# Performance work log

Hardware: AMD Instinct MI355X
Metric: run time of the kernel (lower is better)

The kernel has to match this reference:

```python
import jax, jax.numpy as jnp
import numpy as np

B, N, D, E = 256, 192, 512, 1024
H = E // 2          # MLP hidden = 512
K = 58              # round(0.3 * 192), hardcoded in the torch forward
EPS_L2 = 1e-8
EPS_BN = 1e-5


def setup_inputs() -> dict:
    key = jax.random.key(0)
    ks = jax.random.split(key, 8)
    s = 0.02
    return {
        "all_patch_embeddings": jax.random.normal(ks[0], (B, N, D), dtype=jnp.float32),
        "attention_map": jax.random.uniform(ks[1], (B, N + 1, N + 1), dtype=jnp.float32),
        # fc: Linear(D, E)
        "W_fc": jax.random.normal(ks[2], (E, D), dtype=jnp.float32) * s,
        "b_fc": jnp.zeros((E,), dtype=jnp.float32),
        # mlp layer 0: Linear(D, H) + BatchNorm1d(H) + ReLU
        "W1": jax.random.normal(ks[3], (H, D), dtype=jnp.float32) * s,
        "b1": jnp.zeros((H,), dtype=jnp.float32),
        "gamma1": jnp.ones((H,), dtype=jnp.float32),
        "beta1": jnp.zeros((H,), dtype=jnp.float32),
        # mlp layer 1: Linear(H, E) (no BN/ReLU applied on last layer)
        "W2": jax.random.normal(ks[4], (E, H), dtype=jnp.float32) * s,
        "b2": jnp.zeros((E,), dtype=jnp.float32),
    }


def reference(all_patch_embeddings, attention_map, W_fc, b_fc, W1, b1, gamma1, beta1, W2, b2):
    # CLS-row attention over the 192 patch tokens: [B, N]
    cls_attn = attention_map[:, 0, 1:]
    # torch.sort(descending)[...,:K] == top-k indices (batched, replaces python loop)
    _, idx = jax.lax.top_k(cls_attn, K)                      # [B, K] int32
    # batched gather replacing the per-sample index_select loop
    sel = jnp.take_along_axis(all_patch_embeddings, idx[:, :, None], axis=1)  # [B, K, D]
    # l2norm over last dim
    norm = jnp.sqrt(jnp.sum(sel * sel, axis=-1, keepdims=True)) + EPS_L2
    base = sel / norm
    # .half() cast in the original (round-trip to fp16 precision)
    base = base.astype(jnp.float16).astype(jnp.float32)
    # fc branch
    feat_fc = jnp.einsum('bkd,ed->bke', base, W_fc) + b_fc    # [B, K, E]
    # mlp branch (num_layers=2): Linear -> BN(train-mode batch stats) -> ReLU -> Linear
    h = jnp.einsum('bkd,hd->bkh', base, W1) + b1              # [B, K, H]
    hf = h.reshape(B * K, H)
    mu = jnp.mean(hf, axis=0)
    var = jnp.var(hf, axis=0)
    hf = (hf - mu) * jax.lax.rsqrt(var + EPS_BN) * gamma1 + beta1
    h = jax.nn.relu(hf).reshape(B, K, H)
    feat_mlp = jnp.einsum('bkh,eh->bke', h, W2) + b2          # [B, K, E]
    feats = feat_mlp + feat_fc
    # maxk_pool1d_var with k=1 and lengths == K reduces to max over token dim
    return jnp.max(feats, axis=1).astype(jnp.float32)         # [B, E]
```

## Files before the change

kernel.cpp:

```cpp
#include <hip/hip_runtime.h>
#include <hip/hip_fp16.h>

#define B_ 256
#define N_ 192
#define D_ 512
#define E_ 1024
#define H_ 512
#define K_ 58
#define M_ (B_*K_)
#define M2_ (B_*64)

typedef _Float16 f16;
typedef unsigned int u32;
typedef _Float16 half8 __attribute__((ext_vector_type(8)));
typedef float floatx4 __attribute__((ext_vector_type(4)));

__device__ inline half8 cvt8(float4 f0, float4 f1) {
  half8 r;
  r[0]=(f16)f0.x; r[1]=(f16)f0.y; r[2]=(f16)f0.z; r[3]=(f16)f0.w;
  r[4]=(f16)f1.x; r[5]=(f16)f1.y; r[6]=(f16)f1.z; r[7]=(f16)f1.w;
  return r;
}

__device__ inline void gl_lds16(const f16* g, f16* l) {
  __builtin_amdgcn_global_load_lds((const __attribute__((address_space(1))) u32*)g,
                                   (__attribute__((address_space(3))) u32*)l, 16, 0, 0);
}

__device__ inline void stage128(const f16* gbase, int gstride, f16* sT, int w, int lane) {
  int lrow  = lane >> 2;
  int chunk = (lane & 3) ^ ((lane >> 3) & 3);
  gl_lds16(gbase + (size_t)(w*16      + lrow)*gstride + chunk*8, &sT[(w*16)*32]);
  gl_lds16(gbase + (size_t)(64 + w*16 + lrow)*gstride + chunk*8, &sT[(64 + w*16)*32]);
}

__global__ void setup_kernel(const float* __restrict__ Wfc, const float* __restrict__ W2,
                             const float* __restrict__ W1, const float* __restrict__ attn,
                             const float* __restrict__ emb,
                             f16* __restrict__ Wcat, f16* __restrict__ W1_16,
                             f16* __restrict__ A16, float* __restrict__ csum) {
  __shared__ float sv[N_];
  __shared__ int sidx[K_];
  __shared__ int cnt;
  int blk = blockIdx.x, t = threadIdx.x;
  if (blk < 512) {
    int idx = (blk*256 + t)*8;
    int e = idx >> 10, c = idx & 1023;
    const float* src = (c < 512) ? (Wfc + (size_t)e*512 + c)
                                 : (W2  + (size_t)e*512 + (c-512));
    half8 o = cvt8(((const float4*)src)[0], ((const float4*)src)[1]);
    *(uint4*)(Wcat + idx) = *(uint4*)&o;
  } else if (blk < 640) {
    int idx = ((blk-512)*256 + t)*8;
    const float* src = W1 + idx;
    half8 o = cvt8(((const float4*)src)[0], ((const float4*)src)[1]);
    *(uint4*)(W1_16 + idx) = *(uint4*)&o;
  } else if (blk < 896) {
    int b = blk - 640;
    if (t == 0) cnt = 0;
    if (t < N_) sv[t] = attn[(size_t)b*193*193 + 1 + t];
    __syncthreads();
    if (t < N_) {
      float v = sv[t]; int rank = 0;
      for (int j = 0; j < N_; ++j) {
        float vj = sv[j];
        rank += (vj > v) || (vj == v && j < t);
      }
      if (rank < K_) sidx[atomicAdd(&cnt, 1)] = t;
    }
    __syncthreads();
    int w = t >> 6, lane = t & 63;
    for (int slot = w; slot < 64; slot += 4) {
      f16* dst = A16 + ((size_t)b*64 + slot)*1024 + lane*8;
      if (slot < K_) {
        const float* src = emb + ((size_t)b*N_ + sidx[slot])*D_ + lane*8;
        float4 v0 = ((const float4*)src)[0];
        float4 v1 = ((const float4*)src)[1];
        float s = v0.x*v0.x + v0.y*v0.y + v0.z*v0.z + v0.w*v0.w
                + v1.x*v1.x + v1.y*v1.y + v1.z*v1.z + v1.w*v1.w;
        #pragma unroll
        for (int off = 32; off > 0; off >>= 1) s += __shfl_xor(s, off);
        float inv = 1.0f / (sqrtf(s) + 1e-8f);
        half8 o;
        o[0]=(f16)(v0.x*inv); o[1]=(f16)(v0.y*inv); o[2]=(f16)(v0.z*inv); o[3]=(f16)(v0.w*inv);
        o[4]=(f16)(v1.x*inv); o[5]=(f16)(v1.y*inv); o[6]=(f16)(v1.z*inv); o[7]=(f16)(v1.w*inv);
        *(uint4*)dst = *(uint4*)&o;
      } else {
        uint4 z; z.x=0u; z.y=0u; z.z=0u; z.w=0u;
        *(uint4*)dst = z;
      }
    }
  } else {
    float4 z; z.x=0.f; z.y=0.f; z.z=0.f; z.w=0.f;
    ((float4*)csum)[t] = z;
  }
}

__launch_bounds__(256)
__global__ void gemm1_kernel(const f16* __restrict__ A16, const f16* __restrict__ W1_16,
                             const float* __restrict__ b1, f16* __restrict__ Aout,
                             float* __restrict__ csum, float* __restrict__ css) {
  __shared__ f16 sA[128*32];
  __shared__ f16 sB[128*32];
  __shared__ float sSum[4][64], sSS[4][64];
  int t = threadIdx.x;
  int n0 = blockIdx.x * 128;
  int m0 = blockIdx.y * 128;
  int lane = t & 63, w = t >> 6, lm = lane & 15, quad = lane >> 4;
  int rh = w & 1, ch = w >> 1;
  floatx4 acc[4][4] = {};
  const f16* Ab = A16 + (size_t)m0*1024;
  const f16* Bb = W1_16 + (size_t)n0*512;
  int sw = (quad ^ ((lm >> 1) & 3)) * 8;
  for (int k0 = 0; k0 < 512; k0 += 32) {
    stage128(Ab + k0, 1024, sA, w, lane);
    stage128(Bb + k0, 512,  sB, w, lane);
    __syncthreads();
    half8 a[4], bf[4];
    #pragma unroll
    for (int i = 0; i < 4; ++i) a[i]  = *(const half8*)&sA[(rh*64 + i*16 + lm)*32 + sw];
    #pragma unroll
    for (int j = 0; j < 4; ++j) bf[j] = *(const half8*)&sB[(ch*64 + j*16 + lm)*32 + sw];
    #pragma unroll
    for (int i = 0; i < 4; ++i)
      #pragma unroll
      for (int j = 0; j < 4; ++j)
        acc[i][j] = __builtin_amdgcn_mfma_f32_16x16x32_f16(a[i], bf[j], acc[i][j], 0, 0, 0);
    __syncthreads();
  }
  #pragma unroll
  for (int j = 0; j < 4; ++j) {
    int col = n0 + ch*64 + j*16 + lm;
    float bias = b1[col];
    float s = 0.f, ss = 0.f;
    #pragma unroll
    for (int i = 0; i < 4; ++i) {
      int rib = i*16 + quad*4;
      int row = m0 + rh*64 + rib;
      #pragma unroll
      for (int r = 0; r < 4; ++r) {
        float x = acc[i][j][r] + bias;
        Aout[(size_t)(row + r)*1024 + 512 + col] = (f16)x;
        if (rib + r < K_) { s += x; ss += x*x; }
      }
    }
    s  += __shfl_xor(s, 16);  s  += __shfl_xor(s, 32);
    ss += __shfl_xor(ss, 16); ss += __shfl_xor(ss, 32);
    if (lane < 16) { sSum[w][j*16 + lm] = s; sSS[w][j*16 + lm] = ss; }
  }
  __syncthreads();
  if (t < 128) {
    int wp = (t >> 6) * 2, ci = t & 63;
    atomicAdd(&csum[n0 + t], sSum[wp][ci] + sSum[wp+1][ci]);
    atomicAdd(&css[n0 + t],  sSS[wp][ci]  + sSS[wp+1][ci]);
  }
}

__global__ void bnrelu_kernel(f16* __restrict__ A16, const float* __restrict__ csum,
                              const float* __restrict__ css, const float* __restrict__ gamma,
                              const float* __restrict__ beta) {
  __shared__ float sSc[H_], sSh[H_];
  int t = threadIdx.x;
  for (int j = t; j < H_; j += 256) {
    float mu  = csum[j] * (1.0f/M_);
    float var = css[j] * (1.0f/M_) - mu*mu;
    float sc  = gamma[j] * rsqrtf(var + 1e-5f);
    sSc[j] = sc;
    sSh[j] = beta[j] - mu*sc;
  }
  __syncthreads();
  int r0 = blockIdx.x * 16;
  #pragma unroll
  for (int i = 0; i < 4; ++i) {
    int seg = t + 256*i;
    int row = r0 + (seg >> 6);
    int c0  = (seg & 63) * 8;
    f16* p = A16 + (size_t)row*1024 + 512 + c0;
    if ((row & 63) >= K_) {
      uint4 z; z.x=0u; z.y=0u; z.z=0u; z.w=0u;
      *(uint4*)p = z;
    } else {
      half8 hv = *(const half8*)p;
      half8 o;
      #pragma unroll
      for (int k = 0; k < 8; ++k)
        o[k] = (f16)fmaxf((float)hv[k]*sSc[c0+k] + sSh[c0+k], 0.0f);
      *(uint4*)p = *(uint4*)&o;
    }
  }
}

__launch_bounds__(256)
__global__ void fused_kernel(const f16* __restrict__ A16, const f16* __restrict__ Wcat,
                             const float* __restrict__ bfc, const float* __restrict__ b2,
                             float* __restrict__ out) {
  __shared__ f16 sA[128*32];
  __shared__ f16 sB[128*32];
  __shared__ float sMax[4][64];
  int t = threadIdx.x;
  int e0 = blockIdx.x * 128;
  int bm = blockIdx.y;
  int lane = t & 63, w = t >> 6, lm = lane & 15, quad = lane >> 4;
  int rh = w & 1, ch = w >> 1;
  floatx4 acc[4][4] = {};
  const f16* Ab = A16 + (size_t)bm*128*1024;
  const f16* Bb = Wcat + (size_t)e0*1024;
  int sw = (quad ^ ((lm >> 1) & 3)) * 8;
  for (int k0 = 0; k0 < 1024; k0 += 32) {
    stage128(Ab + k0, 1024, sA, w, lane);
    stage128(Bb + k0, 1024, sB, w, lane);
    __syncthreads();
    half8 a[4], bf[4];
    #pragma unroll
    for (int i = 0; i < 4; ++i) a[i]  = *(const half8*)&sA[(rh*64 + i*16 + lm)*32 + sw];
    #pragma unroll
    for (int j = 0; j < 4; ++j) bf[j] = *(const half8*)&sB[(ch*64 + j*16 + lm)*32 + sw];
    #pragma unroll
    for (int i = 0; i < 4; ++i)
      #pragma unroll
      for (int j = 0; j < 4; ++j)
        acc[i][j] = __builtin_amdgcn_mfma_f32_16x16x32_f16(a[i], bf[j], acc[i][j], 0, 0, 0);
    __syncthreads();
  }
  #pragma unroll
  for (int j = 0; j < 4; ++j) {
    float mx = -3.0e38f;
    #pragma unroll
    for (int i = 0; i < 4; ++i) {
      int rib = i*16 + quad*4;
      #pragma unroll
      for (int r = 0; r < 4; ++r)
        if (rib + r < K_) mx = fmaxf(mx, acc[i][j][r]);
    }
    mx = fmaxf(mx, __shfl_xor(mx, 16));
    mx = fmaxf(mx, __shfl_xor(mx, 32));
    if (lane < 16) sMax[w][j*16 + lm] = mx;
  }
  __syncthreads();
  {
    int bb = t >> 7, c = t & 127;
    float mx = sMax[(c >> 6)*2 + bb][c & 63];
    int e = e0 + c;
    out[((size_t)bm*2 + bb)*E_ + e] = mx + bfc[e] + b2[e];
  }
}

extern "C" void kernel_launch(void* const* d_in, const int* in_sizes, int n_in,
                              void* d_out, int out_size, void* d_ws, size_t ws_size,
                              hipStream_t stream) {
  const float* emb   = (const float*)d_in[0];
  const float* attn  = (const float*)d_in[1];
  const float* Wfc   = (const float*)d_in[2];
  const float* bfc   = (const float*)d_in[3];
  const float* W1    = (const float*)d_in[4];
  const float* b1    = (const float*)d_in[5];
  const float* gamma = (const float*)d_in[6];
  const float* beta  = (const float*)d_in[7];
  const float* W2    = (const float*)d_in[8];
  const float* b2    = (const float*)d_in[9];
  float* out = (float*)d_out;

  char* ws = (char*)d_ws;
  f16*   A16   = (f16*)(ws);
  f16*   Wcat  = (f16*)(ws + 33554432);
  f16*   W1_16 = (f16*)(ws + 35651584);
  float* csum  = (float*)(ws + 36175872);
  float* css   = (float*)(ws + 36177920);

  setup_kernel<<<897, 256, 0, stream>>>(Wfc, W2, W1, attn, emb, Wcat, W1_16, A16, csum);
  gemm1_kernel<<<dim3(H_/128, M2_/128), 256, 0, stream>>>(A16, W1_16, b1, A16, csum, css);
  bnrelu_kernel<<<M2_/16, 256, 0, stream>>>(A16, csum, css, gamma, beta);
  fused_kernel<<<dim3(E_/128, M2_/128), 256, 0, stream>>>(A16, Wcat, bfc, b2, out);
}
```

Before: 255.1 us.

## Fuse BN+ReLU into second GEMM and switch to register-prefetched 64-wide K tiles

Removes the separate bnrelu kernel: the second GEMM now computes BN scale/shift per block and applies BN+ReLU (and zeroes padded rows) to the A tile in registers before writing it to LDS. Both GEMMs drop the global_load_lds staging in favour of register prefetch of the next 64-wide K tile, overlapped with MFMA on the current tile, using an XOR-swizzled LDS layout. This saves a full read/write pass over the hidden activations and a kernel launch. In exchange, the BN transform is recomputed by every column block, and register pressure and LDS usage per block increase.

```diff
diff --git a/kernel.cpp b/kernel.cpp
--- a/kernel.cpp
+++ b/kernel.cpp
@@ -11,7 +11,6 @@
 #define M2_ (B_*64)
 
 typedef _Float16 f16;
-typedef unsigned int u32;
 typedef _Float16 half8 __attribute__((ext_vector_type(8)));
 typedef float floatx4 __attribute__((ext_vector_type(4)));
 
@@ -20,18 +19,6 @@
   r[0]=(f16)f0.x; r[1]=(f16)f0.y; r[2]=(f16)f0.z; r[3]=(f16)f0.w;
   r[4]=(f16)f1.x; r[5]=(f16)f1.y; r[6]=(f16)f1.z; r[7]=(f16)f1.w;
   return r;
-}
-
-__device__ inline void gl_lds16(const f16* g, f16* l) {
-  __builtin_amdgcn_global_load_lds((const __attribute__((address_space(1))) u32*)g,
-                                   (__attribute__((address_space(3))) u32*)l, 16, 0, 0);
-}
-
-__device__ inline void stage128(const f16* gbase, int gstride, f16* sT, int w, int lane) {
-  int lrow  = lane >> 2;
-  int chunk = (lane & 3) ^ ((lane >> 3) & 3);
-  gl_lds16(gbase + (size_t)(w*16      + lrow)*gstride + chunk*8, &sT[(w*16)*32]);
-  gl_lds16(gbase + (size_t)(64 + w*16 + lrow)*gstride + chunk*8, &sT[(64 + w*16)*32]);
 }
 
 __global__ void setup_kernel(const float* __restrict__ Wfc, const float* __restrict__ W2,
@@ -100,33 +87,55 @@
 __global__ void gemm1_kernel(const f16* __restrict__ A16, const f16* __restrict__ W1_16,
                              const float* __restrict__ b1, f16* __restrict__ Aout,
                              float* __restrict__ csum, float* __restrict__ css) {
-  __shared__ f16 sA[128*32];
-  __shared__ f16 sB[128*32];
+  __shared__ f16 sA[128*64];
+  __shared__ f16 sB[128*64];
   __shared__ float sSum[4][64], sSS[4][64];
   int t = threadIdx.x;
   int n0 = blockIdx.x * 128;
   int m0 = blockIdx.y * 128;
   int lane = t & 63, w = t >> 6, lm = lane & 15, quad = lane >> 4;
   int rh = w & 1, ch = w >> 1;
+  int tr = t >> 3, tc = (t & 7) * 8;
+  int wslot8 = ((t & 7) ^ (tr & 7)) * 8;
   floatx4 acc[4][4] = {};
   const f16* Ab = A16 + (size_t)m0*1024;
   const f16* Bb = W1_16 + (size_t)n0*512;
-  int sw = (quad ^ ((lm >> 1) & 3)) * 8;
-  for (int k0 = 0; k0 < 512; k0 += 32) {
-    stage128(Ab + k0, 1024, sA, w, lane);
-    stage128(Bb + k0, 512,  sB, w, lane);
-    __syncthreads();
-    half8 a[4], bf[4];
-    #pragma unroll
-    for (int i = 0; i < 4; ++i) a[i]  = *(const half8*)&sA[(rh*64 + i*16 + lm)*32 + sw];
-    #pragma unroll
-    for (int j = 0; j < 4; ++j) bf[j] = *(const half8*)&sB[(ch*64 + j*16 + lm)*32 + sw];
-    #pragma unroll
-    for (int i = 0; i < 4; ++i)
-      #pragma unroll
-      for (int j = 0; j < 4; ++j)
-        acc[i][j] = __builtin_amdgcn_mfma_f32_16x16x32_f16(a[i], bf[j], acc[i][j], 0, 0, 0);
-    __syncthreads();
+  uint4 rA[4], rB[4];
+  #pragma unroll
+  for (int i = 0; i < 4; ++i) {
+    rA[i] = *(const uint4*)(Ab + (size_t)(i*32 + tr)*1024 + tc);
+    rB[i] = *(const uint4*)(Bb + (size_t)(i*32 + tr)*512  + tc);
+  }
+  for (int it = 0; it < 8; ++it) {
+    __syncthreads();
+    #pragma unroll
+    for (int i = 0; i < 4; ++i) {
+      *(uint4*)&sA[(i*32 + tr)*64 + wslot8] = rA[i];
+      *(uint4*)&sB[(i*32 + tr)*64 + wslot8] = rB[i];
+    }
+    __syncthreads();
+    if (it < 7) {
+      int kn = it*64 + 64;
+      #pragma unroll
+      for (int i = 0; i < 4; ++i) {
+        rA[i] = *(const uint4*)(Ab + (size_t)(i*32 + tr)*1024 + kn + tc);
+        rB[i] = *(const uint4*)(Bb + (size_t)(i*32 + tr)*512  + kn + tc);
+      }
+    }
+    #pragma unroll
+    for (int ksub = 0; ksub < 2; ++ksub) {
+      int ko = ((quad + 4*ksub) ^ (lm & 7)) * 8;
+      half8 a[4], bf[4];
+      #pragma unroll
+      for (int i = 0; i < 4; ++i) a[i]  = *(const half8*)&sA[(rh*64 + i*16 + lm)*64 + ko];
+      #pragma unroll
+      for (int j = 0; j < 4; ++j) bf[j] = *(const half8*)&sB[(ch*64 + j*16 + lm)*64 + ko];
+      #pragma unroll
+      for (int i = 0; i < 4; ++i)
+        #pragma unroll
+        for (int j = 0; j < 4; ++j)
+          acc[i][j] = __builtin_amdgcn_mfma_f32_16x16x32_f16(a[i], bf[j], acc[i][j], 0, 0, 0);
+    }
   }
   #pragma unroll
   for (int j = 0; j < 4; ++j) {
@@ -156,71 +165,92 @@
   }
 }
 
-__global__ void bnrelu_kernel(f16* __restrict__ A16, const float* __restrict__ csum,
-                              const float* __restrict__ css, const float* __restrict__ gamma,
-                              const float* __restrict__ beta) {
-  __shared__ float sSc[H_], sSh[H_];
-  int t = threadIdx.x;
-  for (int j = t; j < H_; j += 256) {
-    float mu  = csum[j] * (1.0f/M_);
-    float var = css[j] * (1.0f/M_) - mu*mu;
-    float sc  = gamma[j] * rsqrtf(var + 1e-5f);
-    sSc[j] = sc;
-    sSh[j] = beta[j] - mu*sc;
-  }
-  __syncthreads();
-  int r0 = blockIdx.x * 16;
-  #pragma unroll
-  for (int i = 0; i < 4; ++i) {
-    int seg = t + 256*i;
-    int row = r0 + (seg >> 6);
-    int c0  = (seg & 63) * 8;
-    f16* p = A16 + (size_t)row*1024 + 512 + c0;
-    if ((row & 63) >= K_) {
-      uint4 z; z.x=0u; z.y=0u; z.z=0u; z.w=0u;
-      *(uint4*)p = z;
-    } else {
-      half8 hv = *(const half8*)p;
-      half8 o;
-      #pragma unroll
-      for (int k = 0; k < 8; ++k)
-        o[k] = (f16)fmaxf((float)hv[k]*sSc[c0+k] + sSh[c0+k], 0.0f);
-      *(uint4*)p = *(uint4*)&o;
-    }
-  }
-}
-
 __launch_bounds__(256)
 __global__ void fused_kernel(const f16* __restrict__ A16, const f16* __restrict__ Wcat,
+                             const float* __restrict__ csum, const float* __restrict__ css,
+                             const float* __restrict__ gamma, const float* __restrict__ beta,
                              const float* __restrict__ bfc, const float* __restrict__ b2,
                              float* __restrict__ out) {
-  __shared__ f16 sA[128*32];
-  __shared__ f16 sB[128*32];
+  __shared__ f16 sA[128*64];
+  __shared__ f16 sB[128*64];
+  __shared__ float sSc[H_], sSh[H_];
   __shared__ float sMax[4][64];
   int t = threadIdx.x;
   int e0 = blockIdx.x * 128;
   int bm = blockIdx.y;
   int lane = t & 63, w = t >> 6, lm = lane & 15, quad = lane >> 4;
   int rh = w & 1, ch = w >> 1;
+  int tr = t >> 3, tc = (t & 7) * 8;
+  int wslot8 = ((t & 7) ^ (tr & 7)) * 8;
+  #pragma unroll
+  for (int jj = 0; jj < 2; ++jj) {
+    int j = t + jj*256;
+    float mu  = csum[j] * (1.0f/M_);
+    float var = css[j] * (1.0f/M_) - mu*mu;
+    float sc  = gamma[j] * rsqrtf(var + 1e-5f);
+    sSc[j] = sc;
+    sSh[j] = beta[j] - mu*sc;
+  }
   floatx4 acc[4][4] = {};
   const f16* Ab = A16 + (size_t)bm*128*1024;
   const f16* Bb = Wcat + (size_t)e0*1024;
-  int sw = (quad ^ ((lm >> 1) & 3)) * 8;
-  for (int k0 = 0; k0 < 1024; k0 += 32) {
-    stage128(Ab + k0, 1024, sA, w, lane);
-    stage128(Bb + k0, 1024, sB, w, lane);
-    __syncthreads();
-    half8 a[4], bf[4];
-    #pragma unroll
-    for (int i = 0; i < 4; ++i) a[i]  = *(const half8*)&sA[(rh*64 + i*16 + lm)*32 + sw];
-    #pragma unroll
-    for (int j = 0; j < 4; ++j) bf[j] = *(const half8*)&sB[(ch*64 + j*16 + lm)*32 + sw];
-    #pragma unroll
-    for (int i = 0; i < 4; ++i)
-      #pragma unroll
-      for (int j = 0; j < 4; ++j)
-        acc[i][j] = __builtin_amdgcn_mfma_f32_16x16x32_f16(a[i], bf[j], acc[i][j], 0, 0, 0);
-    __syncthreads();
+  uint4 rA[4], rB[4];
+  #pragma unroll
+  for (int i = 0; i < 4; ++i) {
+    rA[i] = *(const uint4*)(Ab + (size_t)(i*32 + tr)*1024 + tc);
+    rB[i] = *(const uint4*)(Bb + (size_t)(i*32 + tr)*1024 + tc);
+  }
+  for (int it = 0; it < 16; ++it) {
+    int k0 = it*64;
+    __syncthreads();
+    if (k0 >= 512) {
+      int cb = k0 - 512 + tc;
+      float4 sc0 = *(float4*)&sSc[cb], sc1 = *(float4*)&sSc[cb+4];
+      float4 sh0 = *(float4*)&sSh[cb], sh1 = *(float4*)&sSh[cb+4];
+      #pragma unroll
+      for (int i = 0; i < 4; ++i) {
+        half8 hv = *(half8*)&rA[i];
+        half8 o;
+        o[0]=(f16)fmaxf((float)hv[0]*sc0.x+sh0.x, 0.f);
+        o[1]=(f16)fmaxf((float)hv[1]*sc0.y+sh0.y, 0.f);
+        o[2]=(f16)fmaxf((float)hv[2]*sc0.z+sh0.z, 0.f);
+        o[3]=(f16)fmaxf((float)hv[3]*sc0.w+sh0.w, 0.f);
+        o[4]=(f16)fmaxf((float)hv[4]*sc1.x+sh1.x, 0.f);
+        o[5]=(f16)fmaxf((float)hv[5]*sc1.y+sh1.y, 0.f);
+        o[6]=(f16)fmaxf((float)hv[6]*sc1.z+sh1.z, 0.f);
+        o[7]=(f16)fmaxf((float)hv[7]*sc1.w+sh1.w, 0.f);
+        if ((i & 1) && ((t >> 3) >= 26)) { uint4 z; z.x=0u;z.y=0u;z.z=0u;z.w=0u; rA[i] = z; }
+        else rA[i] = *(uint4*)&o;
+      }
+    }
+    #pragma unroll
+    for (int i = 0; i < 4; ++i) {
+      *(uint4*)&sA[(i*32 + tr)*64 + wslot8] = rA[i];
+      *(uint4*)&sB[(i*32 + tr)*64 + wslot8] = rB[i];
+    }
+    __syncthreads();
+    if (it < 15) {
+      int kn = k0 + 64;
+      #pragma unroll
+      for (int i = 0; i < 4; ++i) {
+        rA[i] = *(const uint4*)(Ab + (size_t)(i*32 + tr)*1024 + kn + tc);
+        rB[i] = *(const uint4*)(Bb + (size_t)(i*32 + tr)*1024 + kn + tc);
+      }
+    }
+    #pragma unroll
+    for (int ksub = 0; ksub < 2; ++ksub) {
+      int ko = ((quad + 4*ksub) ^ (lm & 7)) * 8;
+      half8 a[4], bf[4];
+      #pragma unroll
+      for (int i = 0; i < 4; ++i) a[i]  = *(const half8*)&sA[(rh*64 + i*16 + lm)*64 + ko];
+      #pragma unroll
+      for (int j = 0; j < 4; ++j) bf[j] = *(const half8*)&sB[(ch*64 + j*16 + lm)*64 + ko];
+      #pragma unroll
+      for (int i = 0; i < 4; ++i)
+        #pragma unroll
+        for (int j = 0; j < 4; ++j)
+          acc[i][j] = __builtin_amdgcn_mfma_f32_16x16x32_f16(a[i], bf[j], acc[i][j], 0, 0, 0);
+    }
   }
   #pragma unroll
   for (int j = 0; j < 4; ++j) {
@@ -269,6 +299,6 @@
 
   setup_kernel<<<897, 256, 0, stream>>>(Wfc, W2, W1, attn, emb, Wcat, W1_16, A16, csum);
   gemm1_kernel<<<dim3(H_/128, M2_/128), 256, 0, stream>>>(A16, W1_16, b1, A16, csum, css);
-  bnrelu_kernel<<<M2_/16, 256, 0, stream>>>(A16, csum, css, gamma, beta);
-  fused_kernel<<<dim3(E_/128, M2_/128), 256, 0, stream>>>(A16, Wcat, bfc, b2, out);
-}
+  fused_kernel<<<dim3(E_/128, M2_/128), 256, 0, stream>>>(A16, Wcat, csum, css, gamma, beta,
+                                                          bfc, b2, out);
+}
```

After: 316.5 us. 24.0% more time.
